# Kernel optimization log

Measured on AMD Instinct MI355X. Metric: run time of the kernel, lower is better.

## Reference

```python
import jax, jax.numpy as jnp
import numpy as np

B = 8192
FL = 96      # feature_len
K = 3        # dynamic filter kernel size
NOUT = 2
EPS = 1e-5
P = (K - 1) // 2

def _lrelu(x):
    return jnp.where(x >= 0, x, 0.1 * x)

def _conv1d(x, w, b):
    # x: [b,1,L], w: [1,1,3], b: [1]; padding=1, stride=1
    y = jax.lax.conv_general_dilated(x, w, (1,), [(1, 1)], dimension_numbers=('NCH', 'OIH', 'NCH'))
    return y + b[None, :, None]

def _bn(y, g, be, m, v):
    # eval-mode BatchNorm1d with running stats
    return (y - m) / jnp.sqrt(v + EPS) * g + be


def setup_inputs() -> dict:
    key = jax.random.key(0)
    ks = jax.random.split(key, 40)
    d = {'x': jax.random.normal(ks[0], (B, 576), jnp.float32)}
    # trans_layer: 6 conv1d (1->1, k=3)
    for i in range(6):
        d[f'cw{i+1}'] = jax.random.normal(ks[1 + i], (1, 1, 3), jnp.float32) * 0.4
        d[f'cb{i+1}'] = jax.random.normal(ks[7 + i], (1,), jnp.float32) * 0.1
    # fusion_layer.de_dimen: Linear(FL -> K*K)
    d['de_W'] = jax.random.normal(ks[13], (K * K, FL), jnp.float32) * 0.1
    d['de_b'] = jnp.zeros((K * K,), jnp.float32)
    # reshape_layer: Linear(2*FL -> 3*FL) + BN
    d['rs_W'] = jax.random.normal(ks[14], (3 * FL, 2 * FL), jnp.float32) * 0.07
    d['rs_b'] = jnp.zeros((3 * FL,), jnp.float32)
    d['rs_g'] = 1.0 + 0.1 * jax.random.normal(ks[15], (3 * FL,), jnp.float32)
    d['rs_be'] = 0.1 * jax.random.normal(ks[16], (3 * FL,), jnp.float32)
    d['rs_m'] = 0.05 * jax.random.normal(ks[17], (3 * FL,), jnp.float32)
    d['rs_v'] = jax.random.uniform(ks[18], (3 * FL,), jnp.float32, 0.5, 1.5)
    # classifier_shallow: Linear(6*FL -> 3*FL) + BN + ReLU + Linear(3*FL -> NOUT)
    d['cl_W1'] = jax.random.normal(ks[19], (3 * FL, 6 * FL), jnp.float32) * 0.05
    d['cl_b1'] = jnp.zeros((3 * FL,), jnp.float32)
    d['cl_g'] = 1.0 + 0.1 * jax.random.normal(ks[20], (3 * FL,), jnp.float32)
    d['cl_be'] = 0.1 * jax.random.normal(ks[21], (3 * FL,), jnp.float32)
    d['cl_m'] = 0.05 * jax.random.normal(ks[22], (3 * FL,), jnp.float32)
    d['cl_v'] = jax.random.uniform(ks[23], (3 * FL,), jnp.float32, 0.5, 1.5)
    d['cl_W2'] = jax.random.normal(ks[24], (NOUT, 3 * FL), jnp.float32) * 0.05
    d['cl_b2'] = jnp.zeros((NOUT,), jnp.float32)
    return d


def reference(x, cw1, cb1, cw2, cb2, cw3, cb3, cw4, cb4, cw5, cb5, cw6, cb6,
              de_W, de_b, rs_W, rs_b, rs_g, rs_be, rs_m, rs_v,
              cl_W1, cl_b1, cl_g, cl_be, cl_m, cl_v, cl_W2, cl_b2):
    def trans(c):  # c: [b,1,3*FL] -> three [b,1,FL]
        s1, s2, s3 = c[..., :FL], c[..., FL:2 * FL], c[..., 2 * FL:]
        x1 = _lrelu(_conv1d(s1, cw1, cb1))
        x2 = _lrelu(_conv1d(s2, cw2, cb2))
        x3 = _lrelu(_conv1d(s3, cw3, cb3))
        return (_lrelu(_conv1d(x1, cw4, cb4)),
                _lrelu(_conv1d(x2, cw5, cb5)),
                _lrelu(_conv1d(x3, cw6, cb6)))

    def fusion(arm, x86, bert):  # each [b,1,FL]
        b = arm.shape[0]
        # c==1 so matmul(s_1^T, s_2) is a per-sample outer product: [b,FL,FL]
        m = _lrelu(jnp.einsum('bl,bm->blm', arm[:, 0], x86[:, 0]))
        # per-sample 3x3 dynamic filter from bert embedding
        s3 = _lrelu(bert[:, 0] @ de_W.T + de_b).reshape(b, 1, K, K)
        fe = jax.lax.conv_general_dilated(
            m.reshape(1, b, FL, FL), s3, (1, 1), [(P, P), (P, P)],
            feature_group_count=b, dimension_numbers=('NCHW', 'OIHW', 'NCHW'))
        fe = _lrelu(fe).reshape(b, FL, FL)
        # AvgPool1d(FL) == mean over last dim (and over rows for the permuted map)
        return jnp.concatenate([fe.mean(axis=2), fe.mean(axis=1)], axis=1)  # [b,2*FL]

    def resh(e):
        return _lrelu(_bn(e @ rs_W.T + rs_b, rs_g, rs_be, rs_m, rs_v))

    xu = x[:, None, :]  # unsqueeze(dim=1)
    c1, c2 = xu[..., :3 * FL], xu[..., 3 * FL:]
    e1 = resh(fusion(*trans(c1))) + c1[:, 0]
    e2 = resh(fusion(*trans(c2))) + c2[:, 0]
    ce = jnp.concatenate([e1, e2], axis=1)  # [b,6*FL]
    # Dropout is identity in eval mode
    h = jax.nn.relu(_bn(ce @ cl_W1.T + cl_b1, cl_g, cl_be, cl_m, cl_v))
    return h @ cl_W2.T + cl_b2  # [b,NOUT]
```

## Files before the change

### kernel.cpp

```cpp
#include <hip/hip_runtime.h>
#include <hip/hip_bf16.h>
#include <math.h>

#define FLn 96
#define SEG 288
#define EPRE_DIM 192
#define EPS_BN 1e-5f

typedef __attribute__((ext_vector_type(8))) short short8;
typedef __attribute__((ext_vector_type(4))) float floatx4;
typedef float v2f __attribute__((ext_vector_type(2)));

__device__ __forceinline__ float lrelu(float v) { return fmaxf(v, 0.1f * v); }
__device__ __forceinline__ short f2bf(float f) {
  __hip_bfloat16 h = __float2bfloat16(f);
  return *reinterpret_cast<short*>(&h);
}

#define O_CIN 0
#define O_ST1 288
#define O_APP 576
#define O_ANP 674
#define O_XPP 772
#define O_XNP 870
#define O_BERT 968
#define O_WKER 1064
#define O_ABF 0
#define O_BBF 384
#define O_RP 0
#define RPREG 1632
#define SLICE 3264

__global__ __launch_bounds__(128) void k1_persample(
    const float* __restrict__ x,
    const float* __restrict__ cw1, const float* __restrict__ cb1,
    const float* __restrict__ cw2, const float* __restrict__ cb2,
    const float* __restrict__ cw3, const float* __restrict__ cb3,
    const float* __restrict__ cw4, const float* __restrict__ cb4,
    const float* __restrict__ cw5, const float* __restrict__ cb5,
    const float* __restrict__ cw6, const float* __restrict__ cb6,
    const float* __restrict__ deW, const float* __restrict__ deb,
    const float* __restrict__ rsW, const float* __restrict__ clW1,
    short* __restrict__ wB2s, short* __restrict__ wB3s,
    short* __restrict__ epre_s) {
  __shared__ float S[SLICE];
  short* Ssh = (short*)S;
  const int tid = threadIdx.x;
  const int sw = tid >> 6;
  const int lane = tid & 63;
  const int quad = lane >> 4;
  const int l16 = lane & 15;
  const int unit = blockIdx.x;
  const float* xrow = x + (size_t)(unit >> 1) * 576 + (unit & 1) * 288;

  {
    int d = blockIdx.x * 128 + tid;
    if (d < 18 * 6 * 512) {
      int j = d & 7, ln = (d >> 3) & 63, t = d >> 9;
      int kf = t % 6, nf = t / 6;
      int n = nf * 16 + (ln & 15);
      int k = kf * 32 + (ln >> 4) * 8 + j;
      wB2s[d] = f2bf(rsW[n * 192 + k]);
    }
    if (d < 18 * 18 * 512) {
      int j = d & 7, ln = (d >> 3) & 63, t = d >> 9;
      int kf = t % 18, nt = t / 18;
      int n = nt * 16 + (ln & 15);
      int k = kf * 32 + (ln >> 4) * 8 + j;
      wB3s[d] = f2bf(clW1[n * 576 + k]);
    }
  }

  const float a0w0 = cw1[0], a0w1 = cw1[1], a0w2 = cw1[2], a0b = cb1[0];
  const float a1w0 = cw2[0], a1w1 = cw2[1], a1w2 = cw2[2], a1b = cb2[0];
  const float a2w0 = cw3[0], a2w1 = cw3[1], a2w2 = cw3[2], a2b = cb3[0];
  const float b0w0 = cw4[0], b0w1 = cw4[1], b0w2 = cw4[2], b0b = cb4[0];
  const float b1w0 = cw5[0], b1w1 = cw5[1], b1w2 = cw5[2], b1b = cb5[0];
  const float b2w0 = cw6[0], b2w1 = cw6[1], b2w2 = cw6[2], b2b = cb6[0];

  for (int t4 = tid; t4 < 72; t4 += 128)
    *(float4*)&S[O_CIN + 4 * t4] = ((const float4*)xrow)[t4];
  if (tid < 8) S[576 + 98 * (tid >> 1) + (tid & 1) * 97] = 0.f;
  __syncthreads();

  for (int t = tid; t < SEG; t += 128) {
    bool g1 = t >= 96, g2 = t >= 192;
    float wa = g2 ? a2w0 : (g1 ? a1w0 : a0w0);
    float wb = g2 ? a2w1 : (g1 ? a1w1 : a0w1);
    float wc = g2 ? a2w2 : (g1 ? a1w2 : a0w2);
    float bb = g2 ? a2b  : (g1 ? a1b  : a0b);
    int p = t - (g2 ? 192 : (g1 ? 96 : 0));
    float l = p > 0 ? S[O_CIN + t - 1] : 0.f;
    float m = S[O_CIN + t];
    float r = p < FLn - 1 ? S[O_CIN + t + 1] : 0.f;
    S[O_ST1 + t] = lrelu(fmaf(wa, l, fmaf(wb, m, fmaf(wc, r, bb))));
  }
  __syncthreads();
  for (int t = tid; t < SEG; t += 128) {
    bool g1 = t >= 96, g2 = t >= 192;
    float wa = g2 ? b2w0 : (g1 ? b1w0 : b0w0);
    float wb = g2 ? b2w1 : (g1 ? b1w1 : b0w1);
    float wc = g2 ? b2w2 : (g1 ? b1w2 : b0w2);
    float bb = g2 ? b2b  : (g1 ? b1b  : b0b);
    int p = t - (g2 ? 192 : (g1 ? 96 : 0));
    float l = p > 0 ? S[O_ST1 + t - 1] : 0.f;
    float m = S[O_ST1 + t];
    float r = p < FLn - 1 ? S[O_ST1 + t + 1] : 0.f;
    float v = lrelu(fmaf(wa, l, fmaf(wb, m, fmaf(wc, r, bb))));
    if (!g1) {
      S[O_APP + 1 + p] = fmaxf(v, 0.1f * v);
      S[O_ANP + 1 + p] = fminf(v, 0.1f * v);
    } else if (!g2) {
      S[O_XPP + 1 + p] = fmaxf(v, 0.f);
      S[O_XNP + 1 + p] = fminf(v, 0.f);
    } else {
      S[O_BERT + p] = v;
    }
  }
  __syncthreads();

  if (sw == 0) {
    if (quad < 3) {
      float bv[6];
#pragma unroll
      for (int k = 0; k < 6; ++k) bv[k] = S[O_BERT + l16 + 16 * k];
#pragma unroll
      for (int oi = 0; oi < 3; ++oi) {
        int o = quad * 3 + oi;
        float p = 0.f;
#pragma unroll
        for (int k = 0; k < 6; ++k) p = fmaf(bv[k], deW[o * 96 + l16 + 16 * k], p);
        p += __shfl_xor(p, 1, 16);
        p += __shfl_xor(p, 2, 16);
        p += __shfl_xor(p, 4, 16);
        p += __shfl_xor(p, 8, 16);
        if (l16 == 0) S[O_WKER + o] = lrelu(p + deb[o]);
      }
    }
  } else {
    for (int m = lane; m < 96; m += 64) {
      short8 a;
      a[0] = f2bf(S[O_APP + m]);
      a[1] = f2bf(S[O_APP + m + 1]);
      a[2] = f2bf(S[O_APP + m + 2]);
      a[3] = f2bf(S[O_ANP + m]);
      a[4] = f2bf(S[O_ANP + m + 1]);
      a[5] = f2bf(S[O_ANP + m + 2]);
      a[6] = 0; a[7] = 0;
      *(short8*)&Ssh[2 * O_ABF + m * 8] = a;
    }
  }
  __syncthreads();

  {
    float w9[9];
#pragma unroll
    for (int q = 0; q < 9; ++q) w9[q] = 0.25f * S[O_WKER + q];
    for (int t = tid; t < 96; t += 128) {
      float xp0 = S[O_XPP + t], xp1 = S[O_XPP + t + 1], xp2 = S[O_XPP + t + 2];
      float xn0 = S[O_XNP + t], xn1 = S[O_XNP + t + 1], xn2 = S[O_XNP + t + 2];
      short8 b;
#pragma unroll
      for (int d = 0; d < 3; ++d) {
        float cp = fmaf(w9[3 * d], xp0, fmaf(w9[3 * d + 1], xp1, w9[3 * d + 2] * xp2));
        float cn = fmaf(w9[3 * d], xn0, fmaf(w9[3 * d + 1], xn1, w9[3 * d + 2] * xn2));
        b[d] = f2bf(cp);
        b[3 + d] = f2bf(cn);
      }
      b[6] = 0; b[7] = 0;
      *(short8*)&Ssh[2 * O_BBF + t * 8] = b;
    }
  }
  __syncthreads();

  short8 aF[6];
#pragma unroll
  for (int mt = 0; mt < 6; ++mt)
    aF[mt] = *(const short8*)&Ssh[2 * O_ABF + (mt * 16 + l16) * 8];

  v2f rp2[6][2];
#pragma unroll
  for (int mt = 0; mt < 6; ++mt) {
    rp2[mt][0] = (v2f){0.f, 0.f};
    rp2[mt][1] = (v2f){0.f, 0.f};
  }
  float cs[3];

#pragma unroll
  for (int si = 0; si < 3; ++si) {
    const int s = 3 * sw + si;
    short8 bF = *(const short8*)&Ssh[2 * O_BBF + (s * 16 + l16) * 8];
    floatx4 accv[6];
#pragma unroll
    for (int mt = 0; mt < 6; ++mt)
      accv[mt] = __builtin_amdgcn_mfma_f32_16x16x32_bf16(
          aF[mt], bF, (floatx4){0.f, 0.f, 0.f, 0.f}, 0, 0, 0);
    v2f csl = (v2f){0.f, 0.f};
#pragma unroll
    for (int mt = 0; mt < 6; ++mt) {
      v2f lo = (v2f){accv[mt][0], accv[mt][1]};
      v2f hi = (v2f){accv[mt][2], accv[mt][3]};
      v2f tl = 0.1f * lo;
      v2f th = 0.1f * hi;
      v2f fl, fh;
      fl.x = fmaxf(lo.x, tl.x); fl.y = fmaxf(lo.y, tl.y);
      fh.x = fmaxf(hi.x, th.x); fh.y = fmaxf(hi.y, th.y);
      rp2[mt][0] += fl;
      rp2[mt][1] += fh;
      csl += fl + fh;
    }
    cs[si] = csl.x + csl.y;
  }
  __syncthreads();

#pragma unroll
  for (int mt = 0; mt < 6; ++mt)
    *(float4*)&S[O_RP + sw * RPREG + (quad * 6 + mt) * 68 + l16 * 4] =
        make_float4(rp2[mt][0].x, rp2[mt][0].y, rp2[mt][1].x, rp2[mt][1].y);
  __syncthreads();

  const int g = unit >> 4;
  const int u15 = unit & 15;
  short* eb = epre_s + (size_t)g * 6 * 512;
  for (int i = tid; i < 96; i += 128) {
    int gg = ((i >> 2) & 3) * 6 + (i >> 4);
    int r = i & 3;
    float s = 0.f;
#pragma unroll
    for (int l = 0; l < 16; ++l)
      s += S[O_RP + gg * 68 + l * 4 + r] + S[O_RP + RPREG + gg * 68 + l * 4 + r];
    int kf = i >> 5, rem = i & 31, q = rem >> 3, j = rem & 7;
    eb[kf * 512 + (q * 16 + u15) * 8 + j] = f2bf(s * (1.f / FLn));
  }
#pragma unroll
  for (int si = 0; si < 3; ++si) {
    float v = cs[si];
    v += __shfl_xor(v, 16, 64);
    v += __shfl_xor(v, 32, 64);
    if (quad == 0) {
      int kidx = 96 + (3 * sw + si) * 16 + l16;
      int kf = kidx >> 5, rem = kidx & 31, q = rem >> 3, j = rem & 7;
      eb[kf * 512 + (q * 16 + u15) * 8 + j] = f2bf(v * (1.f / FLn));
    }
  }
}

__global__ __launch_bounds__(512) void k6_fused_tail(
    const short* __restrict__ epre_s, const short* __restrict__ wB2s,
    const short* __restrict__ wB3s, const float* __restrict__ x,
    const float* __restrict__ rsb, const float* __restrict__ rsg,
    const float* __restrict__ rsbe, const float* __restrict__ rsm,
    const float* __restrict__ rsv,
    const float* __restrict__ clb1, const float* __restrict__ clg,
    const float* __restrict__ clbe, const float* __restrict__ clm,
    const float* __restrict__ clv,
    const float* __restrict__ clW2, const float* __restrict__ clb2,
    float* __restrict__ out) {
  __shared__ short ceT[16 * 584];
  __shared__ float scr[8 * 32];
  const int tid = threadIdx.x;
  const int w = tid >> 6;
  const int lane = tid & 63;
  const int quad = lane >> 4;
  const int l16 = lane & 15;
  const int s0 = blockIdx.x * 16;

  const int mt = w & 1;
  const int ng = w >> 1;
  short8 aF[6];
  {
    const short* arow = epre_s + (size_t)(blockIdx.x * 2 + mt) * 6 * 512 + lane * 8;
#pragma unroll
    for (int kf = 0; kf < 6; ++kf) aF[kf] = *(const short8*)(arow + kf * 512);
  }

  for (int nf = ng; nf < 18; nf += 4) {
    const short* brow = wB2s + (size_t)nf * 6 * 512 + lane * 8;
    floatx4 acc = (floatx4){0.f, 0.f, 0.f, 0.f};
#pragma unroll
    for (int kf = 0; kf < 6; ++kf) {
      short8 bF = *(const short8*)(brow + kf * 512);
      acc = __builtin_amdgcn_mfma_f32_16x16x32_bf16(aF[kf], bF, acc, 0, 0, 0);
    }
    const int n = nf * 16 + l16;
    const float sc = rsg[n] * rsqrtf(rsv[n] + EPS_BN);
    const float vb = rsb[n], mu = rsm[n], vbe = rsbe[n];
#pragma unroll
    for (int r = 0; r < 4; ++r) {
      int um = mt * 16 + quad * 4 + r;
      int trow = um >> 1;
      int cc = (um & 1) * 288 + n;
      float y = acc[r] + vb;
      float o = (y - mu) * sc + vbe;
      float e = lrelu(o) + x[(size_t)(s0 + trow) * 576 + cc];
      ceT[trow * 584 + cc] = f2bf(e);
    }
  }
  __syncthreads();

  float p0[4], p1[4];
#pragma unroll
  for (int r = 0; r < 4; ++r) { p0[r] = 0.f; p1[r] = 0.f; }

  for (int nt = w; nt < 18; nt += 8) {
    const short* brow = wB3s + (size_t)nt * 18 * 512 + lane * 8;
    floatx4 acc = (floatx4){0.f, 0.f, 0.f, 0.f};
#pragma unroll
    for (int kf = 0; kf < 18; ++kf) {
      short8 cF = *(const short8*)&ceT[l16 * 584 + kf * 32 + quad * 8];
      short8 bF = *(const short8*)(brow + kf * 512);
      acc = __builtin_amdgcn_mfma_f32_16x16x32_bf16(cF, bF, acc, 0, 0, 0);
    }
    const int n = nt * 16 + l16;
    const float sc = clg[n] * rsqrtf(clv[n] + EPS_BN);
    const float vb = clb1[n], mu = clm[n], vbe = clbe[n];
    const float w2a = clW2[n], w2b = clW2[288 + n];
#pragma unroll
    for (int r = 0; r < 4; ++r) {
      float y = acc[r] + vb;
      float hh = fmaxf((y - mu) * sc + vbe, 0.f);
      p0[r] = fmaf(hh, w2a, p0[r]);
      p1[r] = fmaf(hh, w2b, p1[r]);
    }
  }
#pragma unroll
  for (int r = 0; r < 4; ++r) {
#pragma unroll
    for (int off = 1; off < 16; off <<= 1) {
      p0[r] += __shfl_xor(p0[r], off, 64);
      p1[r] += __shfl_xor(p1[r], off, 64);
    }
  }
  if (l16 == 0) {
#pragma unroll
    for (int r = 0; r < 4; ++r) {
      scr[w * 32 + (quad * 4 + r) * 2 + 0] = p0[r];
      scr[w * 32 + (quad * 4 + r) * 2 + 1] = p1[r];
    }
  }
  __syncthreads();
  if (tid < 32) {
    int row = tid >> 1, o = tid & 1;
    float s = 0.f;
#pragma unroll
    for (int g = 0; g < 8; ++g) s += scr[g * 32 + row * 2 + o];
    out[(size_t)(s0 + row) * 2 + o] = s + clb2[o];
  }
}

extern "C" void kernel_launch(void* const* d_in, const int* in_sizes, int n_in,
                              void* d_out, int out_size, void* d_ws, size_t ws_size,
                              hipStream_t stream) {
  const float* x   = (const float*)d_in[0];
  const float* cw1 = (const float*)d_in[1];  const float* cb1 = (const float*)d_in[2];
  const float* cw2 = (const float*)d_in[3];  const float* cb2 = (const float*)d_in[4];
  const float* cw3 = (const float*)d_in[5];  const float* cb3 = (const float*)d_in[6];
  const float* cw4 = (const float*)d_in[7];  const float* cb4 = (const float*)d_in[8];
  const float* cw5 = (const float*)d_in[9];  const float* cb5 = (const float*)d_in[10];
  const float* cw6 = (const float*)d_in[11]; const float* cb6 = (const float*)d_in[12];
  const float* deW = (const float*)d_in[13]; const float* deb = (const float*)d_in[14];
  const float* rsW = (const float*)d_in[15]; const float* rsb = (const float*)d_in[16];
  const float* rsg = (const float*)d_in[17]; const float* rsbe = (const float*)d_in[18];
  const float* rsm = (const float*)d_in[19]; const float* rsv = (const float*)d_in[20];
  const float* clW1 = (const float*)d_in[21]; const float* clb1 = (const float*)d_in[22];
  const float* clg = (const float*)d_in[23]; const float* clbe = (const float*)d_in[24];
  const float* clm = (const float*)d_in[25]; const float* clv = (const float*)d_in[26];
  const float* clW2 = (const float*)d_in[27]; const float* clb2 = (const float*)d_in[28];

  short* ws     = (short*)d_ws;
  short* epre_s = ws;
  short* wB2s   = ws + 16384 * 192;
  short* wB3s   = wB2s + 18 * 6 * 512;

  hipLaunchKernelGGL(k1_persample, dim3(16384), dim3(128), 0, stream, x,
                     cw1, cb1, cw2, cb2, cw3, cb3, cw4, cb4, cw5, cb5, cw6, cb6,
                     deW, deb, rsW, clW1, wB2s, wB3s, epre_s);
  hipLaunchKernelGGL(k6_fused_tail, dim3(512), dim3(512), 0, stream,
                     epre_s, wB2s, wB3s, x,
                     rsb, rsg, rsbe, rsm, rsv,
                     clb1, clg, clbe, clm, clv,
                     clW2, clb2, (float*)d_out);
}
```

Before: 193.5 us.

## Process one sample-unit per wavefront to drop block barriers in k1

Restructures k1 so each 64-lane wavefront handles a whole (sample, half) unit in its own LDS slice, with four units per 256-thread block. All __syncthreads calls are removed because each wave only touches its own slice. The row-pooling reduction now uses cross-lane shuffles instead of an LDS scratch pass. The cost is that each wave does all six MFMA strips serially and the filter and A-fragment prep run on one wave instead of being split across two. The code relies on wave-level lockstep for LDS visibility, with no explicit wave barrier or fence.

```diff
diff --git a/kernel.cpp b/kernel.cpp
--- a/kernel.cpp
+++ b/kernel.cpp
@@ -4,7 +4,6 @@
 
 #define FLn 96
 #define SEG 288
-#define EPRE_DIM 192
 #define EPS_BN 1e-5f
 
 typedef __attribute__((ext_vector_type(8))) short short8;
@@ -17,21 +16,19 @@
   return *reinterpret_cast<short*>(&h);
 }
 
-#define O_CIN 0
-#define O_ST1 288
-#define O_APP 576
-#define O_ANP 674
-#define O_XPP 772
-#define O_XNP 870
-#define O_BERT 968
-#define O_WKER 1064
-#define O_ABF 0
-#define O_BBF 384
-#define O_RP 0
-#define RPREG 1632
-#define SLICE 3264
-
-__global__ __launch_bounds__(128) void k1_persample(
+#define U_CIN 0
+#define U_ST1 288
+#define U_APP 576
+#define U_ANP 674
+#define U_XPP 772
+#define U_XNP 870
+#define U_BERT 968
+#define U_WKER 1064
+#define U_ABF 0
+#define U_BBF 384
+#define USLICE 1088
+
+__global__ __launch_bounds__(256) void k1_persample(
     const float* __restrict__ x,
     const float* __restrict__ cw1, const float* __restrict__ cb1,
     const float* __restrict__ cw2, const float* __restrict__ cb2,
@@ -43,18 +40,19 @@
     const float* __restrict__ rsW, const float* __restrict__ clW1,
     short* __restrict__ wB2s, short* __restrict__ wB3s,
     short* __restrict__ epre_s) {
-  __shared__ float S[SLICE];
-  short* Ssh = (short*)S;
+  __shared__ float S_all[4 * USLICE];
   const int tid = threadIdx.x;
-  const int sw = tid >> 6;
+  const int w = tid >> 6;
   const int lane = tid & 63;
   const int quad = lane >> 4;
   const int l16 = lane & 15;
-  const int unit = blockIdx.x;
+  const int unit = blockIdx.x * 4 + w;
+  float* S = S_all + w * USLICE;
+  short* Ssh = (short*)S;
   const float* xrow = x + (size_t)(unit >> 1) * 576 + (unit & 1) * 288;
 
   {
-    int d = blockIdx.x * 128 + tid;
+    int d = blockIdx.x * 256 + tid;
     if (d < 18 * 6 * 512) {
       int j = d & 7, ln = (d >> 3) & 63, t = d >> 9;
       int kf = t % 6, nf = t / 6;
@@ -78,87 +76,81 @@
   const float b1w0 = cw5[0], b1w1 = cw5[1], b1w2 = cw5[2], b1b = cb5[0];
   const float b2w0 = cw6[0], b2w1 = cw6[1], b2w2 = cw6[2], b2b = cb6[0];
 
-  for (int t4 = tid; t4 < 72; t4 += 128)
-    *(float4*)&S[O_CIN + 4 * t4] = ((const float4*)xrow)[t4];
-  if (tid < 8) S[576 + 98 * (tid >> 1) + (tid & 1) * 97] = 0.f;
-  __syncthreads();
-
-  for (int t = tid; t < SEG; t += 128) {
+  for (int t4 = lane; t4 < 72; t4 += 64)
+    *(float4*)&S[U_CIN + 4 * t4] = ((const float4*)xrow)[t4];
+  if (lane < 8) S[U_APP + 98 * (lane >> 1) + (lane & 1) * 97] = 0.f;
+
+  for (int t = lane; t < SEG; t += 64) {
     bool g1 = t >= 96, g2 = t >= 192;
     float wa = g2 ? a2w0 : (g1 ? a1w0 : a0w0);
     float wb = g2 ? a2w1 : (g1 ? a1w1 : a0w1);
     float wc = g2 ? a2w2 : (g1 ? a1w2 : a0w2);
     float bb = g2 ? a2b  : (g1 ? a1b  : a0b);
     int p = t - (g2 ? 192 : (g1 ? 96 : 0));
-    float l = p > 0 ? S[O_CIN + t - 1] : 0.f;
-    float m = S[O_CIN + t];
-    float r = p < FLn - 1 ? S[O_CIN + t + 1] : 0.f;
-    S[O_ST1 + t] = lrelu(fmaf(wa, l, fmaf(wb, m, fmaf(wc, r, bb))));
-  }
-  __syncthreads();
-  for (int t = tid; t < SEG; t += 128) {
+    float l = p > 0 ? S[U_CIN + t - 1] : 0.f;
+    float m = S[U_CIN + t];
+    float r = p < FLn - 1 ? S[U_CIN + t + 1] : 0.f;
+    S[U_ST1 + t] = lrelu(fmaf(wa, l, fmaf(wb, m, fmaf(wc, r, bb))));
+  }
+  for (int t = lane; t < SEG; t += 64) {
     bool g1 = t >= 96, g2 = t >= 192;
     float wa = g2 ? b2w0 : (g1 ? b1w0 : b0w0);
     float wb = g2 ? b2w1 : (g1 ? b1w1 : b0w1);
     float wc = g2 ? b2w2 : (g1 ? b1w2 : b0w2);
     float bb = g2 ? b2b  : (g1 ? b1b  : b0b);
     int p = t - (g2 ? 192 : (g1 ? 96 : 0));
-    float l = p > 0 ? S[O_ST1 + t - 1] : 0.f;
-    float m = S[O_ST1 + t];
-    float r = p < FLn - 1 ? S[O_ST1 + t + 1] : 0.f;
+    float l = p > 0 ? S[U_ST1 + t - 1] : 0.f;
+    float m = S[U_ST1 + t];
+    float r = p < FLn - 1 ? S[U_ST1 + t + 1] : 0.f;
     float v = lrelu(fmaf(wa, l, fmaf(wb, m, fmaf(wc, r, bb))));
     if (!g1) {
-      S[O_APP + 1 + p] = fmaxf(v, 0.1f * v);
-      S[O_ANP + 1 + p] = fminf(v, 0.1f * v);
+      S[U_APP + 1 + p] = fmaxf(v, 0.1f * v);
+      S[U_ANP + 1 + p] = fminf(v, 0.1f * v);
     } else if (!g2) {
-      S[O_XPP + 1 + p] = fmaxf(v, 0.f);
-      S[O_XNP + 1 + p] = fminf(v, 0.f);
+      S[U_XPP + 1 + p] = fmaxf(v, 0.f);
+      S[U_XNP + 1 + p] = fminf(v, 0.f);
     } else {
-      S[O_BERT + p] = v;
-    }
-  }
-  __syncthreads();
-
-  if (sw == 0) {
-    if (quad < 3) {
-      float bv[6];
-#pragma unroll
-      for (int k = 0; k < 6; ++k) bv[k] = S[O_BERT + l16 + 16 * k];
-#pragma unroll
-      for (int oi = 0; oi < 3; ++oi) {
-        int o = quad * 3 + oi;
-        float p = 0.f;
-#pragma unroll
-        for (int k = 0; k < 6; ++k) p = fmaf(bv[k], deW[o * 96 + l16 + 16 * k], p);
-        p += __shfl_xor(p, 1, 16);
-        p += __shfl_xor(p, 2, 16);
-        p += __shfl_xor(p, 4, 16);
-        p += __shfl_xor(p, 8, 16);
-        if (l16 == 0) S[O_WKER + o] = lrelu(p + deb[o]);
-      }
-    }
-  } else {
-    for (int m = lane; m < 96; m += 64) {
-      short8 a;
-      a[0] = f2bf(S[O_APP + m]);
-      a[1] = f2bf(S[O_APP + m + 1]);
-      a[2] = f2bf(S[O_APP + m + 2]);
-      a[3] = f2bf(S[O_ANP + m]);
-      a[4] = f2bf(S[O_ANP + m + 1]);
-      a[5] = f2bf(S[O_ANP + m + 2]);
-      a[6] = 0; a[7] = 0;
-      *(short8*)&Ssh[2 * O_ABF + m * 8] = a;
-    }
-  }
-  __syncthreads();
+      S[U_BERT + p] = v;
+    }
+  }
+
+  if (quad < 3) {
+    float bv[6];
+#pragma unroll
+    for (int k = 0; k < 6; ++k) bv[k] = S[U_BERT + l16 + 16 * k];
+#pragma unroll
+    for (int oi = 0; oi < 3; ++oi) {
+      int o = quad * 3 + oi;
+      float p = 0.f;
+#pragma unroll
+      for (int k = 0; k < 6; ++k) p = fmaf(bv[k], deW[o * 96 + l16 + 16 * k], p);
+      p += __shfl_xor(p, 1, 16);
+      p += __shfl_xor(p, 2, 16);
+      p += __shfl_xor(p, 4, 16);
+      p += __shfl_xor(p, 8, 16);
+      if (l16 == 0) S[U_WKER + o] = lrelu(p + deb[o]);
+    }
+  }
+
+  for (int m = lane; m < 96; m += 64) {
+    short8 a;
+    a[0] = f2bf(S[U_APP + m]);
+    a[1] = f2bf(S[U_APP + m + 1]);
+    a[2] = f2bf(S[U_APP + m + 2]);
+    a[3] = f2bf(S[U_ANP + m]);
+    a[4] = f2bf(S[U_ANP + m + 1]);
+    a[5] = f2bf(S[U_ANP + m + 2]);
+    a[6] = 0; a[7] = 0;
+    *(short8*)&Ssh[2 * U_ABF + m * 8] = a;
+  }
 
   {
     float w9[9];
 #pragma unroll
-    for (int q = 0; q < 9; ++q) w9[q] = 0.25f * S[O_WKER + q];
-    for (int t = tid; t < 96; t += 128) {
-      float xp0 = S[O_XPP + t], xp1 = S[O_XPP + t + 1], xp2 = S[O_XPP + t + 2];
-      float xn0 = S[O_XNP + t], xn1 = S[O_XNP + t + 1], xn2 = S[O_XNP + t + 2];
+    for (int q = 0; q < 9; ++q) w9[q] = 0.25f * S[U_WKER + q];
+    for (int t = lane; t < 96; t += 64) {
+      float xp0 = S[U_XPP + t], xp1 = S[U_XPP + t + 1], xp2 = S[U_XPP + t + 2];
+      float xn0 = S[U_XNP + t], xn1 = S[U_XNP + t + 1], xn2 = S[U_XNP + t + 2];
       short8 b;
 #pragma unroll
       for (int d = 0; d < 3; ++d) {
@@ -168,15 +160,14 @@
         b[3 + d] = f2bf(cn);
       }
       b[6] = 0; b[7] = 0;
-      *(short8*)&Ssh[2 * O_BBF + t * 8] = b;
-    }
-  }
-  __syncthreads();
+      *(short8*)&Ssh[2 * U_BBF + t * 8] = b;
+    }
+  }
 
   short8 aF[6];
 #pragma unroll
   for (int mt = 0; mt < 6; ++mt)
-    aF[mt] = *(const short8*)&Ssh[2 * O_ABF + (mt * 16 + l16) * 8];
+    aF[mt] = *(const short8*)&Ssh[2 * U_ABF + (mt * 16 + l16) * 8];
 
   v2f rp2[6][2];
 #pragma unroll
@@ -184,12 +175,14 @@
     rp2[mt][0] = (v2f){0.f, 0.f};
     rp2[mt][1] = (v2f){0.f, 0.f};
   }
-  float cs[3];
-
-#pragma unroll
-  for (int si = 0; si < 3; ++si) {
-    const int s = 3 * sw + si;
-    short8 bF = *(const short8*)&Ssh[2 * O_BBF + (s * 16 + l16) * 8];
+
+  const int g = unit >> 4;
+  const int u15 = unit & 15;
+  short* eb = epre_s + (size_t)g * 3072;
+
+#pragma unroll
+  for (int s = 0; s < 6; ++s) {
+    short8 bF = *(const short8*)&Ssh[2 * U_BBF + (s * 16 + l16) * 8];
     floatx4 accv[6];
 #pragma unroll
     for (int mt = 0; mt < 6; ++mt)
@@ -209,38 +202,35 @@
       rp2[mt][1] += fh;
       csl += fl + fh;
     }
-    cs[si] = csl.x + csl.y;
-  }
-  __syncthreads();
-
-#pragma unroll
-  for (int mt = 0; mt < 6; ++mt)
-    *(float4*)&S[O_RP + sw * RPREG + (quad * 6 + mt) * 68 + l16 * 4] =
-        make_float4(rp2[mt][0].x, rp2[mt][0].y, rp2[mt][1].x, rp2[mt][1].y);
-  __syncthreads();
-
-  const int g = unit >> 4;
-  const int u15 = unit & 15;
-  short* eb = epre_s + (size_t)g * 6 * 512;
-  for (int i = tid; i < 96; i += 128) {
-    int gg = ((i >> 2) & 3) * 6 + (i >> 4);
-    int r = i & 3;
-    float s = 0.f;
-#pragma unroll
-    for (int l = 0; l < 16; ++l)
-      s += S[O_RP + gg * 68 + l * 4 + r] + S[O_RP + RPREG + gg * 68 + l * 4 + r];
-    int kf = i >> 5, rem = i & 31, q = rem >> 3, j = rem & 7;
-    eb[kf * 512 + (q * 16 + u15) * 8 + j] = f2bf(s * (1.f / FLn));
-  }
-#pragma unroll
-  for (int si = 0; si < 3; ++si) {
-    float v = cs[si];
-    v += __shfl_xor(v, 16, 64);
-    v += __shfl_xor(v, 32, 64);
+    float c = csl.x + csl.y;
+    c += __shfl_xor(c, 16, 64);
+    c += __shfl_xor(c, 32, 64);
     if (quad == 0) {
-      int kidx = 96 + (3 * sw + si) * 16 + l16;
+      int kidx = 96 + s * 16 + l16;
       int kf = kidx >> 5, rem = kidx & 31, q = rem >> 3, j = rem & 7;
-      eb[kf * 512 + (q * 16 + u15) * 8 + j] = f2bf(v * (1.f / FLn));
+      eb[kf * 512 + (q * 16 + u15) * 8 + j] = f2bf(c * (1.f / FLn));
+    }
+  }
+
+#pragma unroll
+  for (int mt = 0; mt < 6; ++mt) {
+    float r0 = rp2[mt][0].x, r1 = rp2[mt][0].y;
+    float r2 = rp2[mt][1].x, r3 = rp2[mt][1].y;
+#pragma unroll
+    for (int off = 1; off < 16; off <<= 1) {
+      r0 += __shfl_xor(r0, off, 64);
+      r1 += __shfl_xor(r1, off, 64);
+      r2 += __shfl_xor(r2, off, 64);
+      r3 += __shfl_xor(r3, off, 64);
+    }
+    if (l16 == 0) {
+      float vr[4] = {r0, r1, r2, r3};
+#pragma unroll
+      for (int r = 0; r < 4; ++r) {
+        int i = mt * 16 + quad * 4 + r;
+        int kf = i >> 5, rem = i & 31, q = rem >> 3, j = rem & 7;
+        eb[kf * 512 + (q * 16 + u15) * 8 + j] = f2bf(vr[r] * (1.f / FLn));
+      }
     }
   }
 }
@@ -372,7 +362,7 @@
   short* wB2s   = ws + 16384 * 192;
   short* wB3s   = wB2s + 18 * 6 * 512;
 
-  hipLaunchKernelGGL(k1_persample, dim3(16384), dim3(128), 0, stream, x,
+  hipLaunchKernelGGL(k1_persample, dim3(4096), dim3(256), 0, stream, x,
                      cw1, cb1, cw2, cb2, cw3, cb3, cw4, cb4, cw5, cb5, cw6, cb6,
                      deW, deb, rsW, clW1, wB2s, wB3s, epre_s);
   hipLaunchKernelGGL(k6_fused_tail, dim3(512), dim3(512), 0, stream,
```

Measured after the change: 208.2 us. +7.6%, slower.

## Reduce row partials with wave shuffles and remap block-to-sample order

Applied to the files above, without the earlier changes.

The row-sum partials are now reduced across the 16 lanes of each group with xor shuffles. Only the per-wave totals go to a small LDS region, so the large per-lane scratch buffer is gone. This shrinks shared memory per block from about 13KB to 5KB, which can raise occupancy, and removes one barrier plus the strided 16-term LDS summation. The block index is also remapped so that consecutive blocks handle samples 2048 apart, which changes memory locality and ordering across blocks. The shuffle chains add some instructions per lane.

```diff
diff --git a/kernel.cpp b/kernel.cpp
--- a/kernel.cpp
+++ b/kernel.cpp
@@ -4,7 +4,6 @@
 
 #define FLn 96
 #define SEG 288
-#define EPRE_DIM 192
 #define EPS_BN 1e-5f
 
 typedef __attribute__((ext_vector_type(8))) short short8;
@@ -27,9 +26,8 @@
 #define O_WKER 1064
 #define O_ABF 0
 #define O_BBF 384
-#define O_RP 0
-#define RPREG 1632
-#define SLICE 3264
+#define O_RPC 1080
+#define SLICE 1280
 
 __global__ __launch_bounds__(128) void k1_persample(
     const float* __restrict__ x,
@@ -50,7 +48,7 @@
   const int lane = tid & 63;
   const int quad = lane >> 4;
   const int l16 = lane & 15;
-  const int unit = blockIdx.x;
+  const int unit = (blockIdx.x & 7) * 2048 + (blockIdx.x >> 3);
   const float* xrow = x + (size_t)(unit >> 1) * 576 + (unit & 1) * 288;
 
   {
@@ -211,37 +209,44 @@
     }
     cs[si] = csl.x + csl.y;
   }
-  __syncthreads();
-
-#pragma unroll
-  for (int mt = 0; mt < 6; ++mt)
-    *(float4*)&S[O_RP + sw * RPREG + (quad * 6 + mt) * 68 + l16 * 4] =
-        make_float4(rp2[mt][0].x, rp2[mt][0].y, rp2[mt][1].x, rp2[mt][1].y);
-  __syncthreads();
 
   const int g = unit >> 4;
   const int u15 = unit & 15;
-  short* eb = epre_s + (size_t)g * 6 * 512;
-  for (int i = tid; i < 96; i += 128) {
-    int gg = ((i >> 2) & 3) * 6 + (i >> 4);
-    int r = i & 3;
-    float s = 0.f;
-#pragma unroll
-    for (int l = 0; l < 16; ++l)
-      s += S[O_RP + gg * 68 + l * 4 + r] + S[O_RP + RPREG + gg * 68 + l * 4 + r];
-    int kf = i >> 5, rem = i & 31, q = rem >> 3, j = rem & 7;
-    eb[kf * 512 + (q * 16 + u15) * 8 + j] = f2bf(s * (1.f / FLn));
-  }
+  short* eb = epre_s + (size_t)g * 3072;
+
 #pragma unroll
   for (int si = 0; si < 3; ++si) {
-    float v = cs[si];
-    v += __shfl_xor(v, 16, 64);
-    v += __shfl_xor(v, 32, 64);
+    float c = cs[si];
+    c += __shfl_xor(c, 16, 64);
+    c += __shfl_xor(c, 32, 64);
     if (quad == 0) {
       int kidx = 96 + (3 * sw + si) * 16 + l16;
       int kf = kidx >> 5, rem = kidx & 31, q = rem >> 3, j = rem & 7;
-      eb[kf * 512 + (q * 16 + u15) * 8 + j] = f2bf(v * (1.f / FLn));
-    }
+      eb[kf * 512 + (q * 16 + u15) * 8 + j] = f2bf(c * (1.f / FLn));
+    }
+  }
+
+#pragma unroll
+  for (int mt = 0; mt < 6; ++mt) {
+    float r0 = rp2[mt][0].x, r1 = rp2[mt][0].y;
+    float r2 = rp2[mt][1].x, r3 = rp2[mt][1].y;
+#pragma unroll
+    for (int off = 1; off < 16; off <<= 1) {
+      r0 += __shfl_xor(r0, off, 64);
+      r1 += __shfl_xor(r1, off, 64);
+      r2 += __shfl_xor(r2, off, 64);
+      r3 += __shfl_xor(r3, off, 64);
+    }
+    if (l16 == 0)
+      *(float4*)&S[O_RPC + sw * 96 + mt * 16 + quad * 4] =
+          make_float4(r0, r1, r2, r3);
+  }
+  __syncthreads();
+
+  for (int i = tid; i < 96; i += 128) {
+    float s = S[O_RPC + i] + S[O_RPC + 96 + i];
+    int kf = i >> 5, rem = i & 31, q = rem >> 3, j = rem & 7;
+    eb[kf * 512 + (q * 16 + u15) * 8 + j] = f2bf(s * (1.f / FLn));
   }
 }
 
```

New measurement: 211.9 us. 9.5% more time.

## Process both halves of a sample per block in the per-sample kernel

Applied to the files above, without the earlier changes.

Each 128-thread block of the first kernel now handles two units (both 288-element halves of one input row) instead of one, and the grid is halved. Every stage (conv chain, dynamic-filter projection, bf16 packing, MFMA outer-product conv, pooling) is duplicated over two shared-memory slices, so per-block setup, barriers and parameter loads are spread over twice the work. The dynamic-filter weights are loaded into registers up front instead of inside the reduction. The row-partial reduction now has the two waves accumulate into one buffer in turn rather than each writing its own region, which lets the buffer fit in the smaller per-unit slice. The trade-off is more registers per thread and half as many blocks to hide latency.

```diff
diff --git a/kernel.cpp b/kernel.cpp
--- a/kernel.cpp
+++ b/kernel.cpp
@@ -4,7 +4,6 @@
 
 #define FLn 96
 #define SEG 288
-#define EPRE_DIM 192
 #define EPS_BN 1e-5f
 
 typedef __attribute__((ext_vector_type(8))) short short8;
@@ -25,11 +24,7 @@
 #define O_XNP 870
 #define O_BERT 968
 #define O_WKER 1064
-#define O_ABF 0
-#define O_BBF 384
-#define O_RP 0
-#define RPREG 1632
-#define SLICE 3264
+#define USLICE 1632
 
 __global__ __launch_bounds__(128) void k1_persample(
     const float* __restrict__ x,
@@ -43,15 +38,25 @@
     const float* __restrict__ rsW, const float* __restrict__ clW1,
     short* __restrict__ wB2s, short* __restrict__ wB3s,
     short* __restrict__ epre_s) {
-  __shared__ float S[SLICE];
+  __shared__ float S[2 * USLICE];
   short* Ssh = (short*)S;
   const int tid = threadIdx.x;
   const int sw = tid >> 6;
   const int lane = tid & 63;
   const int quad = lane >> 4;
   const int l16 = lane & 15;
-  const int unit = blockIdx.x;
-  const float* xrow = x + (size_t)(unit >> 1) * 576 + (unit & 1) * 288;
+  const int unitA = blockIdx.x * 2;
+
+  float wd[3][6], db3[3];
+  if (sw == 0 && quad < 3) {
+#pragma unroll
+    for (int oi = 0; oi < 3; ++oi) {
+      db3[oi] = deb[quad * 3 + oi];
+#pragma unroll
+      for (int k = 0; k < 6; ++k)
+        wd[oi][k] = deW[(quad * 3 + oi) * 96 + l16 + 16 * k];
+    }
+  }
 
   {
     int d = blockIdx.x * 128 + tid;
@@ -78,9 +83,17 @@
   const float b1w0 = cw5[0], b1w1 = cw5[1], b1w2 = cw5[2], b1b = cb5[0];
   const float b2w0 = cw6[0], b2w1 = cw6[1], b2w2 = cw6[2], b2b = cb6[0];
 
-  for (int t4 = tid; t4 < 72; t4 += 128)
-    *(float4*)&S[O_CIN + 4 * t4] = ((const float4*)xrow)[t4];
-  if (tid < 8) S[576 + 98 * (tid >> 1) + (tid & 1) * 97] = 0.f;
+  {
+    const float4* xr = (const float4*)(x + (size_t)unitA * 288);
+    for (int t4 = tid; t4 < 144; t4 += 128) {
+      int u = t4 >= 72;
+      *(float4*)&S[u * USLICE + O_CIN + 4 * (t4 - 72 * u)] = xr[t4];
+    }
+  }
+  if (tid < 16) {
+    int u = tid >> 3, r = tid & 7;
+    S[u * USLICE + 576 + 98 * (r >> 1) + (r & 1) * 97] = 0.f;
+  }
   __syncthreads();
 
   for (int t = tid; t < SEG; t += 128) {
@@ -90,10 +103,14 @@
     float wc = g2 ? a2w2 : (g1 ? a1w2 : a0w2);
     float bb = g2 ? a2b  : (g1 ? a1b  : a0b);
     int p = t - (g2 ? 192 : (g1 ? 96 : 0));
-    float l = p > 0 ? S[O_CIN + t - 1] : 0.f;
-    float m = S[O_CIN + t];
-    float r = p < FLn - 1 ? S[O_CIN + t + 1] : 0.f;
-    S[O_ST1 + t] = lrelu(fmaf(wa, l, fmaf(wb, m, fmaf(wc, r, bb))));
+    float lA = p > 0 ? S[O_CIN + t - 1] : 0.f;
+    float mA = S[O_CIN + t];
+    float rA = p < FLn - 1 ? S[O_CIN + t + 1] : 0.f;
+    S[O_ST1 + t] = lrelu(fmaf(wa, lA, fmaf(wb, mA, fmaf(wc, rA, bb))));
+    float lB = p > 0 ? S[USLICE + O_CIN + t - 1] : 0.f;
+    float mB = S[USLICE + O_CIN + t];
+    float rB = p < FLn - 1 ? S[USLICE + O_CIN + t + 1] : 0.f;
+    S[USLICE + O_ST1 + t] = lrelu(fmaf(wa, lB, fmaf(wb, mB, fmaf(wc, rB, bb))));
   }
   __syncthreads();
   for (int t = tid; t < SEG; t += 128) {
@@ -103,38 +120,60 @@
     float wc = g2 ? b2w2 : (g1 ? b1w2 : b0w2);
     float bb = g2 ? b2b  : (g1 ? b1b  : b0b);
     int p = t - (g2 ? 192 : (g1 ? 96 : 0));
-    float l = p > 0 ? S[O_ST1 + t - 1] : 0.f;
-    float m = S[O_ST1 + t];
-    float r = p < FLn - 1 ? S[O_ST1 + t + 1] : 0.f;
-    float v = lrelu(fmaf(wa, l, fmaf(wb, m, fmaf(wc, r, bb))));
+    float lA = p > 0 ? S[O_ST1 + t - 1] : 0.f;
+    float mA = S[O_ST1 + t];
+    float rA = p < FLn - 1 ? S[O_ST1 + t + 1] : 0.f;
+    float vA = lrelu(fmaf(wa, lA, fmaf(wb, mA, fmaf(wc, rA, bb))));
+    float lB = p > 0 ? S[USLICE + O_ST1 + t - 1] : 0.f;
+    float mB = S[USLICE + O_ST1 + t];
+    float rB = p < FLn - 1 ? S[USLICE + O_ST1 + t + 1] : 0.f;
+    float vB = lrelu(fmaf(wa, lB, fmaf(wb, mB, fmaf(wc, rB, bb))));
     if (!g1) {
-      S[O_APP + 1 + p] = fmaxf(v, 0.1f * v);
-      S[O_ANP + 1 + p] = fminf(v, 0.1f * v);
+      S[O_APP + 1 + p] = fmaxf(vA, 0.1f * vA);
+      S[O_ANP + 1 + p] = fminf(vA, 0.1f * vA);
+      S[USLICE + O_APP + 1 + p] = fmaxf(vB, 0.1f * vB);
+      S[USLICE + O_ANP + 1 + p] = fminf(vB, 0.1f * vB);
     } else if (!g2) {
-      S[O_XPP + 1 + p] = fmaxf(v, 0.f);
-      S[O_XNP + 1 + p] = fminf(v, 0.f);
+      S[O_XPP + 1 + p] = fmaxf(vA, 0.f);
+      S[O_XNP + 1 + p] = fminf(vA, 0.f);
+      S[USLICE + O_XPP + 1 + p] = fmaxf(vB, 0.f);
+      S[USLICE + O_XNP + 1 + p] = fminf(vB, 0.f);
     } else {
-      S[O_BERT + p] = v;
+      S[O_BERT + p] = vA;
+      S[USLICE + O_BERT + p] = vB;
     }
   }
   __syncthreads();
 
   if (sw == 0) {
     if (quad < 3) {
-      float bv[6];
-#pragma unroll
-      for (int k = 0; k < 6; ++k) bv[k] = S[O_BERT + l16 + 16 * k];
+      float bvA[6], bvB[6];
+#pragma unroll
+      for (int k = 0; k < 6; ++k) {
+        bvA[k] = S[O_BERT + l16 + 16 * k];
+        bvB[k] = S[USLICE + O_BERT + l16 + 16 * k];
+      }
 #pragma unroll
       for (int oi = 0; oi < 3; ++oi) {
         int o = quad * 3 + oi;
-        float p = 0.f;
-#pragma unroll
-        for (int k = 0; k < 6; ++k) p = fmaf(bv[k], deW[o * 96 + l16 + 16 * k], p);
-        p += __shfl_xor(p, 1, 16);
-        p += __shfl_xor(p, 2, 16);
-        p += __shfl_xor(p, 4, 16);
-        p += __shfl_xor(p, 8, 16);
-        if (l16 == 0) S[O_WKER + o] = lrelu(p + deb[o]);
+        float pA = 0.f, pB = 0.f;
+#pragma unroll
+        for (int k = 0; k < 6; ++k) {
+          pA = fmaf(bvA[k], wd[oi][k], pA);
+          pB = fmaf(bvB[k], wd[oi][k], pB);
+        }
+        pA += __shfl_xor(pA, 1, 16);
+        pA += __shfl_xor(pA, 2, 16);
+        pA += __shfl_xor(pA, 4, 16);
+        pA += __shfl_xor(pA, 8, 16);
+        pB += __shfl_xor(pB, 1, 16);
+        pB += __shfl_xor(pB, 2, 16);
+        pB += __shfl_xor(pB, 4, 16);
+        pB += __shfl_xor(pB, 8, 16);
+        if (l16 == 0) {
+          S[O_WKER + o] = lrelu(pA + db3[oi]);
+          S[USLICE + O_WKER + o] = lrelu(pB + db3[oi]);
+        }
       }
     }
   } else {
@@ -147,101 +186,148 @@
       a[4] = f2bf(S[O_ANP + m + 1]);
       a[5] = f2bf(S[O_ANP + m + 2]);
       a[6] = 0; a[7] = 0;
-      *(short8*)&Ssh[2 * O_ABF + m * 8] = a;
+      *(short8*)&Ssh[m * 8] = a;
+      short8 a2;
+      a2[0] = f2bf(S[USLICE + O_APP + m]);
+      a2[1] = f2bf(S[USLICE + O_APP + m + 1]);
+      a2[2] = f2bf(S[USLICE + O_APP + m + 2]);
+      a2[3] = f2bf(S[USLICE + O_ANP + m]);
+      a2[4] = f2bf(S[USLICE + O_ANP + m + 1]);
+      a2[5] = f2bf(S[USLICE + O_ANP + m + 2]);
+      a2[6] = 0; a2[7] = 0;
+      *(short8*)&Ssh[2 * USLICE + m * 8] = a2;
     }
   }
   __syncthreads();
 
   {
-    float w9[9];
-#pragma unroll
-    for (int q = 0; q < 9; ++q) w9[q] = 0.25f * S[O_WKER + q];
+    float w9A[9], w9B[9];
+#pragma unroll
+    for (int q = 0; q < 9; ++q) {
+      w9A[q] = 0.25f * S[O_WKER + q];
+      w9B[q] = 0.25f * S[USLICE + O_WKER + q];
+    }
     for (int t = tid; t < 96; t += 128) {
       float xp0 = S[O_XPP + t], xp1 = S[O_XPP + t + 1], xp2 = S[O_XPP + t + 2];
       float xn0 = S[O_XNP + t], xn1 = S[O_XNP + t + 1], xn2 = S[O_XNP + t + 2];
-      short8 b;
+      float yp0 = S[USLICE + O_XPP + t], yp1 = S[USLICE + O_XPP + t + 1],
+            yp2 = S[USLICE + O_XPP + t + 2];
+      float yn0 = S[USLICE + O_XNP + t], yn1 = S[USLICE + O_XNP + t + 1],
+            yn2 = S[USLICE + O_XNP + t + 2];
+      short8 bA, bB;
 #pragma unroll
       for (int d = 0; d < 3; ++d) {
-        float cp = fmaf(w9[3 * d], xp0, fmaf(w9[3 * d + 1], xp1, w9[3 * d + 2] * xp2));
-        float cn = fmaf(w9[3 * d], xn0, fmaf(w9[3 * d + 1], xn1, w9[3 * d + 2] * xn2));
-        b[d] = f2bf(cp);
-        b[3 + d] = f2bf(cn);
-      }
-      b[6] = 0; b[7] = 0;
-      *(short8*)&Ssh[2 * O_BBF + t * 8] = b;
-    }
-  }
-  __syncthreads();
-
-  short8 aF[6];
-#pragma unroll
-  for (int mt = 0; mt < 6; ++mt)
-    aF[mt] = *(const short8*)&Ssh[2 * O_ABF + (mt * 16 + l16) * 8];
-
-  v2f rp2[6][2];
-#pragma unroll
-  for (int mt = 0; mt < 6; ++mt) {
-    rp2[mt][0] = (v2f){0.f, 0.f};
-    rp2[mt][1] = (v2f){0.f, 0.f};
-  }
-  float cs[3];
-
-#pragma unroll
-  for (int si = 0; si < 3; ++si) {
-    const int s = 3 * sw + si;
-    short8 bF = *(const short8*)&Ssh[2 * O_BBF + (s * 16 + l16) * 8];
-    floatx4 accv[6];
+        float cpA = fmaf(w9A[3 * d], xp0, fmaf(w9A[3 * d + 1], xp1, w9A[3 * d + 2] * xp2));
+        float cnA = fmaf(w9A[3 * d], xn0, fmaf(w9A[3 * d + 1], xn1, w9A[3 * d + 2] * xn2));
+        bA[d] = f2bf(cpA);
+        bA[3 + d] = f2bf(cnA);
+        float cpB = fmaf(w9B[3 * d], yp0, fmaf(w9B[3 * d + 1], yp1, w9B[3 * d + 2] * yp2));
+        float cnB = fmaf(w9B[3 * d], yn0, fmaf(w9B[3 * d + 1], yn1, w9B[3 * d + 2] * yn2));
+        bB[d] = f2bf(cpB);
+        bB[3 + d] = f2bf(cnB);
+      }
+      bA[6] = 0; bA[7] = 0; bB[6] = 0; bB[7] = 0;
+      *(short8*)&Ssh[2 * 384 + t * 8] = bA;
+      *(short8*)&Ssh[2 * (USLICE + 384) + t * 8] = bB;
+    }
+  }
+  __syncthreads();
+
+  v2f rp[2][6][2];
+  float cs[2][3];
+#pragma unroll
+  for (int u = 0; u < 2; ++u) {
+    short* Su = Ssh + 2 * u * USLICE;
+    short8 aF[6];
 #pragma unroll
     for (int mt = 0; mt < 6; ++mt)
-      accv[mt] = __builtin_amdgcn_mfma_f32_16x16x32_bf16(
-          aF[mt], bF, (floatx4){0.f, 0.f, 0.f, 0.f}, 0, 0, 0);
-    v2f csl = (v2f){0.f, 0.f};
+      aF[mt] = *(const short8*)&Su[(mt * 16 + l16) * 8];
 #pragma unroll
     for (int mt = 0; mt < 6; ++mt) {
-      v2f lo = (v2f){accv[mt][0], accv[mt][1]};
-      v2f hi = (v2f){accv[mt][2], accv[mt][3]};
-      v2f tl = 0.1f * lo;
-      v2f th = 0.1f * hi;
-      v2f fl, fh;
-      fl.x = fmaxf(lo.x, tl.x); fl.y = fmaxf(lo.y, tl.y);
-      fh.x = fmaxf(hi.x, th.x); fh.y = fmaxf(hi.y, th.y);
-      rp2[mt][0] += fl;
-      rp2[mt][1] += fh;
-      csl += fl + fh;
-    }
-    cs[si] = csl.x + csl.y;
-  }
-  __syncthreads();
-
-#pragma unroll
-  for (int mt = 0; mt < 6; ++mt)
-    *(float4*)&S[O_RP + sw * RPREG + (quad * 6 + mt) * 68 + l16 * 4] =
-        make_float4(rp2[mt][0].x, rp2[mt][0].y, rp2[mt][1].x, rp2[mt][1].y);
-  __syncthreads();
-
-  const int g = unit >> 4;
-  const int u15 = unit & 15;
-  short* eb = epre_s + (size_t)g * 6 * 512;
-  for (int i = tid; i < 96; i += 128) {
+      rp[u][mt][0] = (v2f){0.f, 0.f};
+      rp[u][mt][1] = (v2f){0.f, 0.f};
+    }
+#pragma unroll
+    for (int si = 0; si < 3; ++si) {
+      const int s = 3 * sw + si;
+      short8 bF = *(const short8*)&Su[2 * 384 + (s * 16 + l16) * 8];
+      floatx4 accv[6];
+#pragma unroll
+      for (int mt = 0; mt < 6; ++mt)
+        accv[mt] = __builtin_amdgcn_mfma_f32_16x16x32_bf16(
+            aF[mt], bF, (floatx4){0.f, 0.f, 0.f, 0.f}, 0, 0, 0);
+      v2f csl = (v2f){0.f, 0.f};
+#pragma unroll
+      for (int mt = 0; mt < 6; ++mt) {
+        v2f lo = (v2f){accv[mt][0], accv[mt][1]};
+        v2f hi = (v2f){accv[mt][2], accv[mt][3]};
+        v2f tl = 0.1f * lo;
+        v2f th = 0.1f * hi;
+        v2f fl, fh;
+        fl.x = fmaxf(lo.x, tl.x); fl.y = fmaxf(lo.y, tl.y);
+        fh.x = fmaxf(hi.x, th.x); fh.y = fmaxf(hi.y, th.y);
+        rp[u][mt][0] += fl;
+        rp[u][mt][1] += fh;
+        csl += fl + fh;
+      }
+      cs[u][si] = csl.x + csl.y;
+    }
+  }
+
+  short* eb = epre_s + (size_t)(unitA >> 4) * 3072;
+  const int u15A = unitA & 15;
+
+#pragma unroll
+  for (int u = 0; u < 2; ++u) {
+#pragma unroll
+    for (int si = 0; si < 3; ++si) {
+      float c = cs[u][si];
+      c += __shfl_xor(c, 16, 64);
+      c += __shfl_xor(c, 32, 64);
+      if (quad == 0) {
+        int kidx = 96 + (3 * sw + si) * 16 + l16;
+        int kf = kidx >> 5, rem = kidx & 31, q = rem >> 3, j = rem & 7;
+        eb[kf * 512 + (q * 16 + u15A + u) * 8 + j] = f2bf(c * (1.f / FLn));
+      }
+    }
+  }
+
+  __syncthreads();
+  if (sw == 0) {
+#pragma unroll
+    for (int u = 0; u < 2; ++u)
+#pragma unroll
+      for (int mt = 0; mt < 6; ++mt)
+        *(float4*)&S[u * USLICE + (quad * 6 + mt) * 68 + l16 * 4] =
+            make_float4(rp[u][mt][0].x, rp[u][mt][0].y,
+                        rp[u][mt][1].x, rp[u][mt][1].y);
+  }
+  __syncthreads();
+  if (sw == 1) {
+#pragma unroll
+    for (int u = 0; u < 2; ++u)
+#pragma unroll
+      for (int mt = 0; mt < 6; ++mt) {
+        float4* p = (float4*)&S[u * USLICE + (quad * 6 + mt) * 68 + l16 * 4];
+        float4 v = *p;
+        v.x += rp[u][mt][0].x; v.y += rp[u][mt][0].y;
+        v.z += rp[u][mt][1].x; v.w += rp[u][mt][1].y;
+        *p = v;
+      }
+  }
+  __syncthreads();
+
+  for (int idx = tid; idx < 192; idx += 128) {
+    int u = idx >= 96 ? 1 : 0;
+    int i = idx - 96 * u;
     int gg = ((i >> 2) & 3) * 6 + (i >> 4);
     int r = i & 3;
+    const float* rpb = S + u * USLICE;
     float s = 0.f;
 #pragma unroll
-    for (int l = 0; l < 16; ++l)
-      s += S[O_RP + gg * 68 + l * 4 + r] + S[O_RP + RPREG + gg * 68 + l * 4 + r];
+    for (int l = 0; l < 16; ++l) s += rpb[gg * 68 + l * 4 + r];
     int kf = i >> 5, rem = i & 31, q = rem >> 3, j = rem & 7;
-    eb[kf * 512 + (q * 16 + u15) * 8 + j] = f2bf(s * (1.f / FLn));
-  }
-#pragma unroll
-  for (int si = 0; si < 3; ++si) {
-    float v = cs[si];
-    v += __shfl_xor(v, 16, 64);
-    v += __shfl_xor(v, 32, 64);
-    if (quad == 0) {
-      int kidx = 96 + (3 * sw + si) * 16 + l16;
-      int kf = kidx >> 5, rem = kidx & 31, q = rem >> 3, j = rem & 7;
-      eb[kf * 512 + (q * 16 + u15) * 8 + j] = f2bf(v * (1.f / FLn));
-    }
+    eb[kf * 512 + (q * 16 + u15A + u) * 8 + j] = f2bf(s * (1.f / FLn));
   }
 }
 
@@ -372,7 +458,7 @@
   short* wB2s   = ws + 16384 * 192;
   short* wB3s   = wB2s + 18 * 6 * 512;
 
-  hipLaunchKernelGGL(k1_persample, dim3(16384), dim3(128), 0, stream, x,
+  hipLaunchKernelGGL(k1_persample, dim3(8192), dim3(128), 0, stream, x,
                      cw1, cb1, cw2, cb2, cw3, cb3, cw4, cb4, cw5, cb5, cw6, cb6,
                      deW, deb, rsW, clW1, wB2s, wB3s, epre_s);
   hipLaunchKernelGGL(k6_fused_tail, dim3(512), dim3(512), 0, stream,
```

After: 241.3 us. +24.7%, slower.
